# Kernel optimization log

Measured on AMD Instinct MI355X. Metric: run time of the kernel, lower is better.

## Reference

```python
import jax, jax.numpy as jnp
import numpy as np

SUB_NO = 5
T_NO = 201
H_NO = 64
T_DATA = 50000
E_SYN = 2000
I_SYN = 200


def setup_inputs() -> dict:
    key = jax.random.key(0)
    ks = jax.random.split(key, 10)
    k_conv = 1.0 / np.sqrt(2 * T_NO)   # pytorch Conv1d init bound: 1/sqrt(in_ch/groups * k)
    k_ff = 1.0 / np.sqrt(H_NO)
    k_root = 1.0 / np.sqrt(SUB_NO)
    return {
        "S_e": jax.random.uniform(ks[0], (T_DATA, E_SYN), dtype=jnp.float32),
        "S_i": jax.random.uniform(ks[1], (T_DATA, I_SYN), dtype=jnp.float32),
        "temp": jnp.ones((), dtype=jnp.float32),
        "C_syn_e_raw": jnp.ones((SUB_NO, E_SYN), dtype=jnp.float32),
        "C_syn_i_raw": jnp.ones((SUB_NO, I_SYN), dtype=jnp.float32),
        "conv_w": jax.random.uniform(ks[2], (H_NO * SUB_NO, 2, T_NO), jnp.float32, -k_conv, k_conv),
        "conv_b": jax.random.uniform(ks[3], (H_NO * SUB_NO,), jnp.float32, -k_conv, k_conv),
        "ff_w": jax.random.uniform(ks[4], (SUB_NO, H_NO), jnp.float32, -k_ff, k_ff),
        "ff_b": jax.random.uniform(ks[5], (SUB_NO,), jnp.float32, -k_ff, k_ff),
        "root_w": jax.random.uniform(ks[6], (SUB_NO,), jnp.float32, -k_root, k_root),
        "root_b": jax.random.uniform(ks[7], (), jnp.float32, -k_root, k_root),
        "V_o": jax.random.normal(ks[8], (1,), dtype=jnp.float32),
    }


def reference(S_e, S_i, temp, C_syn_e_raw, C_syn_i_raw, conv_w, conv_b,
              ff_w, ff_b, root_w, root_b, V_o):
    T_data = S_e.shape[0]
    # softmax over subunit axis (axis 0) of the synapse->subunit assignment logits
    C_syn_e = jax.nn.softmax(C_syn_e_raw / temp, axis=0)  # (sub, E)
    C_syn_i = jax.nn.softmax(C_syn_i_raw / temp, axis=0)  # (sub, I)
    S_e_group = S_e @ C_syn_e.T  # (T, sub)
    S_i_group = S_i @ C_syn_i.T  # (T, sub)
    # interleave: channel 2s = excit, 2s+1 = inhib  -> (T, 2*sub)
    S = jnp.stack([S_e_group, S_i_group], axis=2).reshape(T_data, 2 * SUB_NO)
    S = S.T[None]  # (1, 2*sub, T)
    conv_out = jax.lax.conv_general_dilated(
        S, conv_w,
        window_strides=(1,),
        padding=[(T_NO // 2, T_NO // 2)],
        feature_group_count=SUB_NO,
        dimension_numbers=("NCH", "OIH", "NCH"),
    ) + conv_b[None, :, None]          # (1, sub*H, T)
    conv_out = conv_out[0].reshape(SUB_NO, H_NO, T_data)  # (sub, H, T)
    # per-subunit Linear(H,1) + LeakyReLU, fused as an einsum
    sub_out = jnp.einsum("sht,sh->ts", conv_out, ff_w) + ff_b  # (T, sub)
    sub_out = jax.nn.leaky_relu(sub_out, 0.01)
    root_out = jax.nn.leaky_relu(sub_out @ root_w + root_b, 0.01) + V_o[0]  # (T,)
    return root_out
```

## Files before the change

kernel.cpp:

```cpp
#include <hip/hip_runtime.h>
#include <math.h>

#define SUB 5
#define TNO 201
#define HNO 64
#define TDATA 50000
#define ESYN 2000
#define ISYN 200
#define PAD (TNO/2)

#define QE (ESYN/4)
#define QI (ISYN/4)
#define CP 21
#define LDSC ((QE+QI)*CP)

__global__ void weff_kernel(const float* __restrict__ conv_w,
                            const float* __restrict__ conv_b,
                            const float* __restrict__ ff_w,
                            const float* __restrict__ ff_b,
                            float* __restrict__ Weff,
                            float* __restrict__ beff) {
    int idx = blockIdx.x * blockDim.x + threadIdx.x;
    if (idx < SUB * 2 * TNO) {
        int s   = idx / (2 * TNO);
        int rem = idx - s * (2 * TNO);
        float acc = 0.f;
        #pragma unroll 8
        for (int h = 0; h < HNO; ++h)
            acc = fmaf(ff_w[s * HNO + h], conv_w[(size_t)(s * HNO + h) * (2 * TNO) + rem], acc);
        Weff[idx] = acc;
    }
    if (idx < SUB) {
        float acc = ff_b[idx];
        for (int h = 0; h < HNO; ++h)
            acc = fmaf(ff_w[idx * HNO + h], conv_b[idx * HNO + h], acc);
        beff[idx] = acc;
    }
}

__global__ __launch_bounds__(256) void group_kernel(
        const float* __restrict__ Se, const float* __restrict__ Si,
        const float* __restrict__ rawE, const float* __restrict__ rawI,
        const float* __restrict__ temp,
        float* __restrict__ Sg) {
    __shared__ float ldsC[LDSC];

    float invT = 1.0f / temp[0];
    for (int j = threadIdx.x; j < ESYN + ISYN; j += blockDim.x) {
        float v[SUB];
        float* dst;
        if (j < ESYN) {
            #pragma unroll
            for (int s = 0; s < SUB; ++s) v[s] = rawE[s * ESYN + j] * invT;
            dst = ldsC + (j >> 2) * CP + (j & 3) * SUB;
        } else {
            int jj = j - ESYN;
            #pragma unroll
            for (int s = 0; s < SUB; ++s) v[s] = rawI[s * ISYN + jj] * invT;
            dst = ldsC + QE * CP + (jj >> 2) * CP + (jj & 3) * SUB;
        }
        float m = fmaxf(fmaxf(fmaxf(v[0], v[1]), fmaxf(v[2], v[3])), v[4]);
        float sum = 0.f;
        #pragma unroll
        for (int s = 0; s < SUB; ++s) { v[s] = expf(v[s] - m); sum += v[s]; }
        float r = 1.0f / sum;
        #pragma unroll
        for (int s = 0; s < SUB; ++s) dst[s] = v[s] * r;
    }
    __syncthreads();

    const float* lE = ldsC;
    const float* lI = ldsC + QE * CP;
    int wave = threadIdx.x >> 6;
    int lane = threadIdx.x & 63;
    int nwaves = (gridDim.x * blockDim.x) >> 6;

    for (int t = blockIdx.x * (blockDim.x >> 6) + wave; t < TDATA; t += nwaves) {
        float aE0 = 0.f, aE1 = 0.f, aE2 = 0.f, aE3 = 0.f, aE4 = 0.f;
        float aI0 = 0.f, aI1 = 0.f, aI2 = 0.f, aI3 = 0.f, aI4 = 0.f;

        const float4* rE = (const float4*)(Se + (size_t)t * ESYN);
        for (int q = lane; q < QE; q += 64) {
            float4 v = rE[q];
            const float* c = lE + q * CP;
            aE0 = fmaf(v.x, c[0],  aE0); aE1 = fmaf(v.x, c[1],  aE1);
            aE2 = fmaf(v.x, c[2],  aE2); aE3 = fmaf(v.x, c[3],  aE3);
            aE4 = fmaf(v.x, c[4],  aE4);
            aE0 = fmaf(v.y, c[5],  aE0); aE1 = fmaf(v.y, c[6],  aE1);
            aE2 = fmaf(v.y, c[7],  aE2); aE3 = fmaf(v.y, c[8],  aE3);
            aE4 = fmaf(v.y, c[9],  aE4);
            aE0 = fmaf(v.z, c[10], aE0); aE1 = fmaf(v.z, c[11], aE1);
            aE2 = fmaf(v.z, c[12], aE2); aE3 = fmaf(v.z, c[13], aE3);
            aE4 = fmaf(v.z, c[14], aE4);
            aE0 = fmaf(v.w, c[15], aE0); aE1 = fmaf(v.w, c[16], aE1);
            aE2 = fmaf(v.w, c[17], aE2); aE3 = fmaf(v.w, c[18], aE3);
            aE4 = fmaf(v.w, c[19], aE4);
        }

        const float4* rI = (const float4*)(Si + (size_t)t * ISYN);
        if (lane < QI) {
            float4 v = rI[lane];
            const float* c = lI + lane * CP;
            aI0 = fmaf(v.x, c[0],  aI0); aI1 = fmaf(v.x, c[1],  aI1);
            aI2 = fmaf(v.x, c[2],  aI2); aI3 = fmaf(v.x, c[3],  aI3);
            aI4 = fmaf(v.x, c[4],  aI4);
            aI0 = fmaf(v.y, c[5],  aI0); aI1 = fmaf(v.y, c[6],  aI1);
            aI2 = fmaf(v.y, c[7],  aI2); aI3 = fmaf(v.y, c[8],  aI3);
            aI4 = fmaf(v.y, c[9],  aI4);
            aI0 = fmaf(v.z, c[10], aI0); aI1 = fmaf(v.z, c[11], aI1);
            aI2 = fmaf(v.z, c[12], aI2); aI3 = fmaf(v.z, c[13], aI3);
            aI4 = fmaf(v.z, c[14], aI4);
            aI0 = fmaf(v.w, c[15], aI0); aI1 = fmaf(v.w, c[16], aI1);
            aI2 = fmaf(v.w, c[17], aI2); aI3 = fmaf(v.w, c[18], aI3);
            aI4 = fmaf(v.w, c[19], aI4);
        }

        #pragma unroll
        for (int m = 32; m > 0; m >>= 1) {
            aE0 += __shfl_xor(aE0, m); aE1 += __shfl_xor(aE1, m);
            aE2 += __shfl_xor(aE2, m); aE3 += __shfl_xor(aE3, m);
            aE4 += __shfl_xor(aE4, m);
            aI0 += __shfl_xor(aI0, m); aI1 += __shfl_xor(aI1, m);
            aI2 += __shfl_xor(aI2, m); aI3 += __shfl_xor(aI3, m);
            aI4 += __shfl_xor(aI4, m);
        }
        if (lane == 0) {
            float* o = Sg + (size_t)t * 10;
            o[0] = aE0; o[1] = aI0; o[2] = aE1; o[3] = aI1;
            o[4] = aE2; o[5] = aI2; o[6] = aE3; o[7] = aI3;
            o[8] = aE4; o[9] = aI4;
        }
    }
}

#define OTILE 256
#define OROWS (OTILE + TNO - 1)
#define OSTR 11

__global__ __launch_bounds__(256) void out_kernel(
        const float* __restrict__ Sg, const float* __restrict__ Weff,
        const float* __restrict__ beff, const float* __restrict__ root_w,
        const float* __restrict__ root_b, const float* __restrict__ V_o,
        float* __restrict__ out) {
    __shared__ float sW[SUB * 2 * TNO];
    __shared__ float sS[OROWS * OSTR];
    __shared__ float sb[SUB], srw[SUB], sc[2];

    int tid = threadIdx.x;
    int t0  = blockIdx.x * OTILE;

    for (int i = tid; i < SUB * 2 * TNO; i += OTILE) sW[i] = Weff[i];
    if (tid < SUB) { sb[tid] = beff[tid]; srw[tid] = root_w[tid]; }
    if (tid == 0)  { sc[0] = root_b[0];   sc[1] = V_o[0]; }

    for (int i = tid; i < OROWS * 10; i += OTILE) {
        int rr = i / 10, ch = i - rr * 10;
        int rg = t0 - PAD + rr;
        sS[rr * OSTR + ch] = (rg >= 0 && rg < TDATA) ? Sg[(size_t)rg * 10 + ch] : 0.f;
    }
    __syncthreads();

    int t = t0 + tid;
    if (t >= TDATA) return;

    float a0 = sb[0], a1 = sb[1], a2 = sb[2], a3 = sb[3], a4 = sb[4];
    #pragma unroll 2
    for (int k = 0; k < TNO; ++k) {
        const float* r = sS + (tid + k) * OSTR;
        a0 = fmaf(r[0], sW[0 * 402 + k], a0); a0 = fmaf(r[1], sW[0 * 402 + 201 + k], a0);
        a1 = fmaf(r[2], sW[1 * 402 + k], a1); a1 = fmaf(r[3], sW[1 * 402 + 201 + k], a1);
        a2 = fmaf(r[4], sW[2 * 402 + k], a2); a2 = fmaf(r[5], sW[2 * 402 + 201 + k], a2);
        a3 = fmaf(r[6], sW[3 * 402 + k], a3); a3 = fmaf(r[7], sW[3 * 402 + 201 + k], a3);
        a4 = fmaf(r[8], sW[4 * 402 + k], a4); a4 = fmaf(r[9], sW[4 * 402 + 201 + k], a4);
    }
    auto lk = [](float x) { return x > 0.f ? x : 0.01f * x; };
    a0 = lk(a0); a1 = lk(a1); a2 = lk(a2); a3 = lk(a3); a4 = lk(a4);
    float root = a0 * srw[0] + a1 * srw[1] + a2 * srw[2] + a3 * srw[3] + a4 * srw[4] + sc[0];
    out[t] = lk(root) + sc[1];
}

extern "C" void kernel_launch(void* const* d_in, const int* in_sizes, int n_in,
                              void* d_out, int out_size, void* d_ws, size_t ws_size,
                              hipStream_t stream) {
    (void)in_sizes; (void)n_in; (void)out_size; (void)ws_size;
    const float* Se     = (const float*)d_in[0];
    const float* Si     = (const float*)d_in[1];
    const float* temp   = (const float*)d_in[2];
    const float* rawE   = (const float*)d_in[3];
    const float* rawI   = (const float*)d_in[4];
    const float* conv_w = (const float*)d_in[5];
    const float* conv_b = (const float*)d_in[6];
    const float* ff_w   = (const float*)d_in[7];
    const float* ff_b   = (const float*)d_in[8];
    const float* root_w = (const float*)d_in[9];
    const float* root_b = (const float*)d_in[10];
    const float* V_o    = (const float*)d_in[11];
    float* out = (float*)d_out;

    float* ws   = (float*)d_ws;
    float* Weff = ws;
    float* beff = ws + 2016;
    float* Sg   = ws + 2048;

    hipLaunchKernelGGL(weff_kernel, dim3(8), dim3(256), 0, stream,
                       conv_w, conv_b, ff_w, ff_b, Weff, beff);
    hipLaunchKernelGGL(group_kernel, dim3(768), dim3(256), 0, stream,
                       Se, Si, rawE, rawI, temp, Sg);
    hipLaunchKernelGGL(out_kernel, dim3((TDATA + OTILE - 1) / OTILE), dim3(256), 0, stream,
                       Sg, Weff, beff, root_w, root_b, V_o, out);
}
```

Before: 620.0 us.

## Process four time rows per wave in grouping and use butterfly fold reduction

```diff
diff --git a/kernel.cpp b/kernel.cpp
--- a/kernel.cpp
+++ b/kernel.cpp
@@ -38,6 +38,34 @@
     }
 }
 
+__device__ inline float elemf(float4 v, int e) {
+    switch (e) { case 0: return v.x; case 1: return v.y; case 2: return v.z; default: return v.w; }
+}
+
+__device__ inline float foldp(float a, float b, int m, int lane) {
+    float send = (lane & m) ? a : b;
+    float recv = __shfl_xor(send, m);
+    return ((lane & m) ? b : a) + recv;
+}
+
+template<int CH0>
+__device__ inline void fma_block(float (&acc)[4][10],
+                                 float4 v0, float4 v1, float4 v2, float4 v3,
+                                 const float* c) {
+    #pragma unroll
+    for (int e = 0; e < 4; ++e) {
+        float a0 = elemf(v0, e), a1 = elemf(v1, e), a2 = elemf(v2, e), a3 = elemf(v3, e);
+        #pragma unroll
+        for (int s = 0; s < 5; ++s) {
+            float w = c[e * 5 + s];
+            acc[0][2 * s + CH0] = fmaf(a0, w, acc[0][2 * s + CH0]);
+            acc[1][2 * s + CH0] = fmaf(a1, w, acc[1][2 * s + CH0]);
+            acc[2][2 * s + CH0] = fmaf(a2, w, acc[2][2 * s + CH0]);
+            acc[3][2 * s + CH0] = fmaf(a3, w, acc[3][2 * s + CH0]);
+        }
+    }
+}
+
 __global__ __launch_bounds__(256) void group_kernel(
         const float* __restrict__ Se, const float* __restrict__ Si,
         const float* __restrict__ rawE, const float* __restrict__ rawI,
@@ -73,110 +101,114 @@
     const float* lI = ldsC + QE * CP;
     int wave = threadIdx.x >> 6;
     int lane = threadIdx.x & 63;
-    int nwaves = (gridDim.x * blockDim.x) >> 6;
-
-    for (int t = blockIdx.x * (blockDim.x >> 6) + wave; t < TDATA; t += nwaves) {
-        float aE0 = 0.f, aE1 = 0.f, aE2 = 0.f, aE3 = 0.f, aE4 = 0.f;
-        float aI0 = 0.f, aI1 = 0.f, aI2 = 0.f, aI3 = 0.f, aI4 = 0.f;
-
-        const float4* rE = (const float4*)(Se + (size_t)t * ESYN);
-        for (int q = lane; q < QE; q += 64) {
-            float4 v = rE[q];
-            const float* c = lE + q * CP;
-            aE0 = fmaf(v.x, c[0],  aE0); aE1 = fmaf(v.x, c[1],  aE1);
-            aE2 = fmaf(v.x, c[2],  aE2); aE3 = fmaf(v.x, c[3],  aE3);
-            aE4 = fmaf(v.x, c[4],  aE4);
-            aE0 = fmaf(v.y, c[5],  aE0); aE1 = fmaf(v.y, c[6],  aE1);
-            aE2 = fmaf(v.y, c[7],  aE2); aE3 = fmaf(v.y, c[8],  aE3);
-            aE4 = fmaf(v.y, c[9],  aE4);
-            aE0 = fmaf(v.z, c[10], aE0); aE1 = fmaf(v.z, c[11], aE1);
-            aE2 = fmaf(v.z, c[12], aE2); aE3 = fmaf(v.z, c[13], aE3);
-            aE4 = fmaf(v.z, c[14], aE4);
-            aE0 = fmaf(v.w, c[15], aE0); aE1 = fmaf(v.w, c[16], aE1);
-            aE2 = fmaf(v.w, c[17], aE2); aE3 = fmaf(v.w, c[18], aE3);
-            aE4 = fmaf(v.w, c[19], aE4);
-        }
-
-        const float4* rI = (const float4*)(Si + (size_t)t * ISYN);
+    int nw   = (gridDim.x * blockDim.x) >> 6;
+    int wid  = blockIdx.x * (blockDim.x >> 6) + wave;
+
+    for (int g = wid; g < TDATA / 4; g += nw) {
+        int t0 = g * 4;
+        float acc[4][10];
+        #pragma unroll
+        for (int r = 0; r < 4; ++r)
+            #pragma unroll
+            for (int c = 0; c < 10; ++c) acc[r][c] = 0.f;
+
+        const float4* R0 = (const float4*)(Se + (size_t)(t0 + 0) * ESYN);
+        const float4* R1 = (const float4*)(Se + (size_t)(t0 + 1) * ESYN);
+        const float4* R2 = (const float4*)(Se + (size_t)(t0 + 2) * ESYN);
+        const float4* R3 = (const float4*)(Se + (size_t)(t0 + 3) * ESYN);
+
+        for (int it = 0; it < 7; ++it) {
+            int q = lane + (it << 6);
+            float4 v0 = R0[q], v1 = R1[q], v2 = R2[q], v3 = R3[q];
+            fma_block<0>(acc, v0, v1, v2, v3, lE + q * CP);
+        }
+        {
+            int q = lane + 448;
+            float4 z = make_float4(0.f, 0.f, 0.f, 0.f);
+            float4 v0 = z, v1 = z, v2 = z, v3 = z;
+            if (q < QE) { v0 = R0[q]; v1 = R1[q]; v2 = R2[q]; v3 = R3[q]; }
+            int qc = (q < QE) ? q : 0;
+            fma_block<0>(acc, v0, v1, v2, v3, lE + qc * CP);
+        }
         if (lane < QI) {
-            float4 v = rI[lane];
-            const float* c = lI + lane * CP;
-            aI0 = fmaf(v.x, c[0],  aI0); aI1 = fmaf(v.x, c[1],  aI1);
-            aI2 = fmaf(v.x, c[2],  aI2); aI3 = fmaf(v.x, c[3],  aI3);
-            aI4 = fmaf(v.x, c[4],  aI4);
-            aI0 = fmaf(v.y, c[5],  aI0); aI1 = fmaf(v.y, c[6],  aI1);
-            aI2 = fmaf(v.y, c[7],  aI2); aI3 = fmaf(v.y, c[8],  aI3);
-            aI4 = fmaf(v.y, c[9],  aI4);
-            aI0 = fmaf(v.z, c[10], aI0); aI1 = fmaf(v.z, c[11], aI1);
-            aI2 = fmaf(v.z, c[12], aI2); aI3 = fmaf(v.z, c[13], aI3);
-            aI4 = fmaf(v.z, c[14], aI4);
-            aI0 = fmaf(v.w, c[15], aI0); aI1 = fmaf(v.w, c[16], aI1);
-            aI2 = fmaf(v.w, c[17], aI2); aI3 = fmaf(v.w, c[18], aI3);
-            aI4 = fmaf(v.w, c[19], aI4);
-        }
-
-        #pragma unroll
-        for (int m = 32; m > 0; m >>= 1) {
-            aE0 += __shfl_xor(aE0, m); aE1 += __shfl_xor(aE1, m);
-            aE2 += __shfl_xor(aE2, m); aE3 += __shfl_xor(aE3, m);
-            aE4 += __shfl_xor(aE4, m);
-            aI0 += __shfl_xor(aI0, m); aI1 += __shfl_xor(aI1, m);
-            aI2 += __shfl_xor(aI2, m); aI3 += __shfl_xor(aI3, m);
-            aI4 += __shfl_xor(aI4, m);
-        }
-        if (lane == 0) {
-            float* o = Sg + (size_t)t * 10;
-            o[0] = aE0; o[1] = aI0; o[2] = aE1; o[3] = aI1;
-            o[4] = aE2; o[5] = aI2; o[6] = aE3; o[7] = aI3;
-            o[8] = aE4; o[9] = aI4;
-        }
-    }
-}
-
-#define OTILE 256
-#define OROWS (OTILE + TNO - 1)
-#define OSTR 11
-
-__global__ __launch_bounds__(256) void out_kernel(
+            const float4* I0 = (const float4*)(Si + (size_t)(t0 + 0) * ISYN);
+            const float4* I1 = (const float4*)(Si + (size_t)(t0 + 1) * ISYN);
+            const float4* I2 = (const float4*)(Si + (size_t)(t0 + 2) * ISYN);
+            const float4* I3 = (const float4*)(Si + (size_t)(t0 + 3) * ISYN);
+            float4 v0 = I0[lane], v1 = I1[lane], v2 = I2[lane], v3 = I3[lane];
+            fma_block<1>(acc, v0, v1, v2, v3, lI + lane * CP);
+        }
+
+        float f1[20], f2[10], f3[5];
+        {
+            const float* a = &acc[0][0];
+            #pragma unroll
+            for (int j = 0; j < 20; ++j) f1[j] = foldp(a[2 * j], a[2 * j + 1], 1, lane);
+            #pragma unroll
+            for (int j = 0; j < 10; ++j) f2[j] = foldp(f1[2 * j], f1[2 * j + 1], 2, lane);
+            #pragma unroll
+            for (int j = 0; j < 5; ++j)  f3[j] = foldp(f2[2 * j], f2[2 * j + 1], 4, lane);
+            #pragma unroll
+            for (int j = 0; j < 5; ++j) {
+                f3[j] += __shfl_xor(f3[j], 8);
+                f3[j] += __shfl_xor(f3[j], 16);
+                f3[j] += __shfl_xor(f3[j], 32);
+            }
+        }
+        if (lane < 8) {
+            #pragma unroll
+            for (int j = 0; j < 5; ++j) {
+                int i = 8 * j + lane;
+                int r = i / 10, c = i - 10 * r;
+                Sg[(size_t)(t0 + r) * 10 + c] = f3[j];
+            }
+        }
+    }
+}
+
+#define OB 128
+#define ORS (OB + TNO - 1)
+
+__global__ __launch_bounds__(128) void out_kernel(
         const float* __restrict__ Sg, const float* __restrict__ Weff,
         const float* __restrict__ beff, const float* __restrict__ root_w,
         const float* __restrict__ root_b, const float* __restrict__ V_o,
         float* __restrict__ out) {
-    __shared__ float sW[SUB * 2 * TNO];
-    __shared__ float sS[OROWS * OSTR];
-    __shared__ float sb[SUB], srw[SUB], sc[2];
+    __shared__ float sS[ORS * 10];
 
     int tid = threadIdx.x;
-    int t0  = blockIdx.x * OTILE;
-
-    for (int i = tid; i < SUB * 2 * TNO; i += OTILE) sW[i] = Weff[i];
-    if (tid < SUB) { sb[tid] = beff[tid]; srw[tid] = root_w[tid]; }
-    if (tid == 0)  { sc[0] = root_b[0];   sc[1] = V_o[0]; }
-
-    for (int i = tid; i < OROWS * 10; i += OTILE) {
-        int rr = i / 10, ch = i - rr * 10;
+    int t0  = blockIdx.x * OB;
+
+    for (int i = tid; i < ORS * 5; i += OB) {
+        int rr = i / 5, p = i - rr * 5;
         int rg = t0 - PAD + rr;
-        sS[rr * OSTR + ch] = (rg >= 0 && rg < TDATA) ? Sg[(size_t)rg * 10 + ch] : 0.f;
+        float2 val = make_float2(0.f, 0.f);
+        if (rg >= 0 && rg < TDATA) val = *(const float2*)(Sg + (size_t)rg * 10 + p * 2);
+        *(float2*)(sS + rr * 10 + p * 2) = val;
     }
     __syncthreads();
 
     int t = t0 + tid;
     if (t >= TDATA) return;
 
-    float a0 = sb[0], a1 = sb[1], a2 = sb[2], a3 = sb[3], a4 = sb[4];
-    #pragma unroll 2
+    float acc[SUB];
+    #pragma unroll
+    for (int s = 0; s < SUB; ++s) acc[s] = beff[s];
+
     for (int k = 0; k < TNO; ++k) {
-        const float* r = sS + (tid + k) * OSTR;
-        a0 = fmaf(r[0], sW[0 * 402 + k], a0); a0 = fmaf(r[1], sW[0 * 402 + 201 + k], a0);
-        a1 = fmaf(r[2], sW[1 * 402 + k], a1); a1 = fmaf(r[3], sW[1 * 402 + 201 + k], a1);
-        a2 = fmaf(r[4], sW[2 * 402 + k], a2); a2 = fmaf(r[5], sW[2 * 402 + 201 + k], a2);
-        a3 = fmaf(r[6], sW[3 * 402 + k], a3); a3 = fmaf(r[7], sW[3 * 402 + 201 + k], a3);
-        a4 = fmaf(r[8], sW[4 * 402 + k], a4); a4 = fmaf(r[9], sW[4 * 402 + 201 + k], a4);
+        const float* r = sS + (tid + k) * 10;
+        #pragma unroll
+        for (int s = 0; s < SUB; ++s) {
+            float2 ei = *(const float2*)(r + 2 * s);
+            acc[s] = fmaf(ei.x, Weff[s * 402 + k],
+                     fmaf(ei.y, Weff[s * 402 + 201 + k], acc[s]));
+        }
     }
     auto lk = [](float x) { return x > 0.f ? x : 0.01f * x; };
-    a0 = lk(a0); a1 = lk(a1); a2 = lk(a2); a3 = lk(a3); a4 = lk(a4);
-    float root = a0 * srw[0] + a1 * srw[1] + a2 * srw[2] + a3 * srw[3] + a4 * srw[4] + sc[0];
-    out[t] = lk(root) + sc[1];
+    float root = root_b[0];
+    #pragma unroll
+    for (int s = 0; s < SUB; ++s) root += lk(acc[s]) * root_w[s];
+    out[t] = lk(root) + V_o[0];
 }
 
 extern "C" void kernel_launch(void* const* d_in, const int* in_sizes, int n_in,
@@ -206,6 +238,6 @@
                        conv_w, conv_b, ff_w, ff_b, Weff, beff);
     hipLaunchKernelGGL(group_kernel, dim3(768), dim3(256), 0, stream,
                        Se, Si, rawE, rawI, temp, Sg);
-    hipLaunchKernelGGL(out_kernel, dim3((TDATA + OTILE - 1) / OTILE), dim3(256), 0, stream,
+    hipLaunchKernelGGL(out_kernel, dim3((TDATA + OB - 1) / OB), dim3(128), 0, stream,
                        Sg, Weff, beff, root_w, root_b, V_o, out);
 }
```

Result: no change. 612.5 us (-1.2%).
